# Optimization experiments

Measured on AMD Instinct MI355X. Metric: run time of the kernel, lower is better.

The kernel has to match this reference:

```python
import jax, jax.numpy as jnp
import numpy as np

B, T, D, UNITS, NUM_OUT = 64, 1024, 256, 256, 32


def setup_inputs() -> dict:
    key = jax.random.key(0)
    k1, k2, k3 = jax.random.split(key, 3)
    inputs = jax.random.normal(k1, (B, T, D), dtype=jnp.float32)
    U = jax.random.normal(k2, (D, 4 * UNITS), dtype=jnp.float32) * 0.05
    W = jax.random.normal(k3, (UNITS, 4 * UNITS), dtype=jnp.float32) * 0.05
    b = jnp.zeros((4 * UNITS,), dtype=jnp.float32)
    return {"inputs": inputs, "U": U, "W": W, "b": b, "num_outputs": NUM_OUT}


def reference(inputs, U, W, b, num_outputs):
    # inputs: [B, T, D]; U: [D, 4u]; W: [u, 4u]; b: [4u]
    Bsz, Tlen, _ = inputs.shape
    units = W.shape[0]
    # Precompute input projection as one batched GEMM (x_t @ U + b for all t)
    xz = jnp.einsum('btd,dk->btk', inputs, U) + b  # [B, T, 4u]

    def step(carry, xz_t):
        h, c = carry
        z = xz_t + h @ W  # [B, 4u]
        z0, z1, z2, z3 = jnp.split(z, 4, axis=1)
        i = jax.nn.sigmoid(z0)
        f = jax.nn.sigmoid(z1)
        c_new = f * c + i * jnp.tanh(z2)
        o = jax.nn.sigmoid(z3)
        h_new = o * jnp.tanh(c_new)
        return (h_new, c_new), h_new

    h0 = jnp.zeros((Bsz, units), dtype=inputs.dtype)
    c0 = jnp.zeros((Bsz, units), dtype=inputs.dtype)
    (_, _), hs = jax.lax.scan(step, (h0, c0), jnp.swapaxes(xz, 0, 1))  # hs: [T, B, u]
    outputs = jnp.swapaxes(hs, 0, 1)[:, Tlen - num_outputs:, :]  # [B, num_outputs, u]
    return outputs
```

## Files before the change

### kernel.cpp

```cpp
#include <hip/hip_runtime.h>
#include <hip/hip_fp16.h>
#include <stdint.h>

#define Bsz 64
#define Tsz 1024
#define Dsz 256
#define UNITSn 256
#define Zdim 1024
#define K2n 128
#define WREG 24
#define WLDS 8

typedef _Float16 half2v __attribute__((ext_vector_type(2)));

__device__ __forceinline__ float dot2acc(uint32_t w, uint32_t h, float acc) {
#if __has_builtin(__builtin_amdgcn_fdot2)
  return __builtin_amdgcn_fdot2(__builtin_bit_cast(half2v, w),
                                __builtin_bit_cast(half2v, h), acc, false);
#else
  __half2 wv = __builtin_bit_cast(__half2, w);
  __half2 hv = __builtin_bit_cast(__half2, h);
  acc = fmaf(__half2float(__low2half(wv)),  __half2float(__low2half(hv)),  acc);
  acc = fmaf(__half2float(__high2half(wv)), __half2float(__high2half(hv)), acc);
  return acc;
#endif
}

__device__ __forceinline__ void dot8(const uint4& w0, const uint4& w1, const uint4& h4,
                                     float& a0, float& a1) {
  a0 = dot2acc(w0.x, h4.x, a0); a0 = dot2acc(w0.y, h4.y, a0);
  a0 = dot2acc(w0.z, h4.z, a0); a0 = dot2acc(w0.w, h4.w, a0);
  a1 = dot2acc(w1.x, h4.x, a1); a1 = dot2acc(w1.y, h4.y, a1);
  a1 = dot2acc(w1.z, h4.z, a1); a1 = dot2acc(w1.w, h4.w, a1);
}

__device__ __forceinline__ float sigm(float x)   { return 1.0f / (1.0f + __expf(-x)); }
__device__ __forceinline__ float tanh_f(float x) { return 1.0f - 2.0f / (__expf(2.0f * x) + 1.0f); }

__global__ void convert_w(const float* __restrict__ W, uint32_t* __restrict__ Wp2) {
  int idx = blockIdx.x * 256 + threadIdx.x;
  if (idx >= Zdim * K2n) return;
  int j = idx >> 7, k2 = idx & 127;
  float w0 = W[(size_t)(2 * k2) * Zdim + j];
  float w1 = W[(size_t)(2 * k2 + 1) * Zdim + j];
  __half2 p = __floats2half2_rn(w0, w1);
  Wp2[idx] = __builtin_bit_cast(uint32_t, p);
}

__global__ __launch_bounds__(256) void proj_gemm(
    const float* __restrict__ x, const float* __restrict__ U,
    const float* __restrict__ bias, float* __restrict__ xz, int t0) {
  __shared__ float At[32][68];
  __shared__ float Bt[32][68];
  const int tid  = threadIdx.x;
  const int n0   = blockIdx.x * 64;
  const int tloc = blockIdx.y;
  const int t    = t0 + tloc;
  const int tm = tid >> 4, tn = tid & 15;
  const int am = tid >> 3, ak = (tid & 7) * 4;
  const int bk = tid >> 4, bn = (tid & 15) * 4;
  const float* xb = x + (size_t)t * Dsz;

  float acc[4][4] = {};
  for (int k0 = 0; k0 < Dsz; k0 += 32) {
    float4 a0 = *(const float4*)(xb + (size_t)am * (Tsz * Dsz) + k0 + ak);
    float4 a1 = *(const float4*)(xb + (size_t)(am + 32) * (Tsz * Dsz) + k0 + ak);
    float4 b0 = *(const float4*)(U + (size_t)(k0 + bk) * Zdim + n0 + bn);
    float4 b1 = *(const float4*)(U + (size_t)(k0 + bk + 16) * Zdim + n0 + bn);
    __syncthreads();
    At[ak + 0][am] = a0.x; At[ak + 1][am] = a0.y; At[ak + 2][am] = a0.z; At[ak + 3][am] = a0.w;
    At[ak + 0][am + 32] = a1.x; At[ak + 1][am + 32] = a1.y; At[ak + 2][am + 32] = a1.z; At[ak + 3][am + 32] = a1.w;
    *(float4*)&Bt[bk][bn]      = b0;
    *(float4*)&Bt[bk + 16][bn] = b1;
    __syncthreads();
#pragma unroll
    for (int kk = 0; kk < 32; kk++) {
      float4 av = *(const float4*)&At[kk][tm * 4];
      float4 bv = *(const float4*)&Bt[kk][tn * 4];
      float a_[4] = {av.x, av.y, av.z, av.w};
      float b_[4] = {bv.x, bv.y, bv.z, bv.w};
#pragma unroll
      for (int i = 0; i < 4; i++)
#pragma unroll
        for (int j = 0; j < 4; j++) acc[i][j] = fmaf(a_[i], b_[j], acc[i][j]);
    }
  }
  float4 bb = *(const float4*)&bias[n0 + tn * 4];
  float bias_[4] = {bb.x, bb.y, bb.z, bb.w};
#pragma unroll
  for (int i = 0; i < 4; i++) {
    float4 o;
    o.x = acc[i][0] + bias_[0]; o.y = acc[i][1] + bias_[1];
    o.z = acc[i][2] + bias_[2]; o.w = acc[i][3] + bias_[3];
    *(float4*)(xz + ((size_t)tloc * 64 + tm * 4 + i) * Zdim + n0 + tn * 4) = o;
  }
}

__global__ __launch_bounds__(512, 2) void lstm_chunk(
    const float* __restrict__ xz, const uint32_t* __restrict__ Wp2,
    float* __restrict__ out, uint4* __restrict__ h_state, float* __restrict__ c_state,
    int t0, int Tc, int n_out) {
  extern __shared__ uint32_t smem[];
  uint32_t* Wl = smem;
  uint4* hq    = (uint4*)(smem + 32768);
  float* zf    = (float*)(smem + 32768 + 256);
  float* zo    = zf + 256;

  const int tid = threadIdx.x;
  const int b   = blockIdx.x;

  const uint4* wp0 = (const uint4*)(Wp2 + (size_t)tid * K2n);
  const uint4* wp1 = (const uint4*)(Wp2 + (size_t)(tid + 512) * K2n);
  uint4 w4[2][WREG];
#pragma unroll
  for (int i = 0; i < WREG; i++) { w4[0][i] = wp0[i]; w4[1][i] = wp1[i]; }
#pragma unroll
  for (int q2 = 0; q2 < WLDS; q2++) {
    *(uint4*)(Wl + (size_t)(q2 * 512 + tid) * 4)          = wp0[WREG + q2];
    *(uint4*)(Wl + (size_t)((WLDS + q2) * 512 + tid) * 4) = wp1[WREG + q2];
  }

  float c = 0.0f;
  if (t0 == 0) {
    if (tid < 64) hq[tid] = make_uint4(0, 0, 0, 0);
  } else {
    if (tid < 32)  hq[tid] = h_state[(size_t)b * 32 + tid];
    if (tid < 256) c = c_state[(size_t)b * 256 + tid];
  }
  __syncthreads();

  const float* xzb = xz + (size_t)b * Zdim;
  float nx0 = xzb[tid];
  float nx1 = xzb[tid + 512];
  for (int tl = 0; tl < Tc; tl++) {
    const int buf = tl & 1;
    float acc0 = nx0, acc1 = nx1;
    if (tl + 1 < Tc) {
      nx0 = xzb[(size_t)(tl + 1) * (Bsz * Zdim) + tid];
      nx1 = xzb[(size_t)(tl + 1) * (Bsz * Zdim) + tid + 512];
    }
    const uint4* hc = hq + buf * 32;
#pragma unroll
    for (int q = 0; q < WREG; q++) {
      uint4 h4 = hc[q];
      dot8(w4[0][q], w4[1][q], h4, acc0, acc1);
    }
#pragma unroll
    for (int q2 = 0; q2 < WLDS; q2++) {
      uint4 h4 = hc[WREG + q2];
      uint4 wa = *(const uint4*)(Wl + (size_t)(q2 * 512 + tid) * 4);
      uint4 wb = *(const uint4*)(Wl + (size_t)((WLDS + q2) * 512 + tid) * 4);
      dot8(wa, wb, h4, acc0, acc1);
    }
    if (tid >= 256) { zf[tid - 256] = acc0; zo[tid - 256] = acc1; }
    __syncthreads();
    if (tid < 256) {
      float ig = sigm(acc0);
      float gg = tanh_f(acc1);
      float fg = sigm(zf[tid]);
      float og = sigm(zo[tid]);
      c = fg * c + ig * gg;
      float hn = og * tanh_f(c);
      int ot = (t0 + tl) - (Tsz - n_out);
      if (ot >= 0) out[((size_t)b * n_out + ot) * UNITSn + tid] = hn;
      ((__half*)(hq + (buf ^ 1) * 32))[tid] = __float2half(hn);
    }
    __syncthreads();
  }
  if (tid < 32)  h_state[(size_t)b * 32 + tid] = hq[(Tc & 1) * 32 + tid];
  if (tid < 256) c_state[(size_t)b * 256 + tid] = c;
}

extern "C" void kernel_launch(void* const* d_in, const int* in_sizes, int n_in,
                              void* d_out, int out_size, void* d_ws, size_t ws_size,
                              hipStream_t stream) {
  const float* x    = (const float*)d_in[0];
  const float* U    = (const float*)d_in[1];
  const float* W    = (const float*)d_in[2];
  const float* bias = (const float*)d_in[3];
  float* out = (float*)d_out;
  const int n_out = out_size / (Bsz * UNITSn);

  uint8_t* ws = (uint8_t*)d_ws;
  uint32_t* Wp2  = (uint32_t*)ws;
  uint4* h_state = (uint4*)(ws + (512u << 10));
  float* c_state = (float*)(ws + (544u << 10));
  float* xz      = (float*)(ws + (1u << 20));

  int Tc = Tsz;
  while (Tc > 1 && (size_t)(1u << 20) + (size_t)Tc * (Bsz * Zdim) * 4 > ws_size) Tc >>= 1;

  convert_w<<<dim3((Zdim * K2n + 255) / 256), dim3(256), 0, stream>>>(W, Wp2);

  const int ldsBytes = (32768 + 256 + 512) * 4;
  hipFuncSetAttribute((const void*)lstm_chunk,
                      hipFuncAttributeMaxDynamicSharedMemorySize, ldsBytes);

  for (int t0 = 0; t0 < Tsz; t0 += Tc) {
    proj_gemm<<<dim3(16, Tc), dim3(256), 0, stream>>>(x, U, bias, xz, t0);
    lstm_chunk<<<dim3(Bsz), dim3(512), ldsBytes, stream>>>(xz, Wp2, out, h_state,
                                                           c_state, t0, Tc, n_out);
  }
}
```

Before: 2.055 ms.

## Split recurrent matvec across K halves with register and global-cached weight tiers

```diff
diff --git a/kernel.cpp b/kernel.cpp
--- a/kernel.cpp
+++ b/kernel.cpp
@@ -7,9 +7,8 @@
 #define Dsz 256
 #define UNITSn 256
 #define Zdim 1024
-#define K2n 128
-#define WREG 24
-#define WLDS 8
+#define QV 12
+#define QG 4
 
 typedef _Float16 half2v __attribute__((ext_vector_type(2)));
 
@@ -26,25 +25,47 @@
 #endif
 }
 
-__device__ __forceinline__ void dot8(const uint4& w0, const uint4& w1, const uint4& h4,
-                                     float& a0, float& a1) {
-  a0 = dot2acc(w0.x, h4.x, a0); a0 = dot2acc(w0.y, h4.y, a0);
-  a0 = dot2acc(w0.z, h4.z, a0); a0 = dot2acc(w0.w, h4.w, a0);
-  a1 = dot2acc(w1.x, h4.x, a1); a1 = dot2acc(w1.y, h4.y, a1);
-  a1 = dot2acc(w1.z, h4.z, a1); a1 = dot2acc(w1.w, h4.w, a1);
+__device__ __forceinline__ float dot4(const uint4& w, const uint4& h, float acc) {
+  acc = dot2acc(w.x, h.x, acc); acc = dot2acc(w.y, h.y, acc);
+  acc = dot2acc(w.z, h.z, acc); acc = dot2acc(w.w, h.w, acc);
+  return acc;
 }
 
 __device__ __forceinline__ float sigm(float x)   { return 1.0f / (1.0f + __expf(-x)); }
 __device__ __forceinline__ float tanh_f(float x) { return 1.0f - 2.0f / (__expf(2.0f * x) + 1.0f); }
 
-__global__ void convert_w(const float* __restrict__ W, uint32_t* __restrict__ Wp2) {
-  int idx = blockIdx.x * 256 + threadIdx.x;
-  if (idx >= Zdim * K2n) return;
-  int j = idx >> 7, k2 = idx & 127;
-  float w0 = W[(size_t)(2 * k2) * Zdim + j];
-  float w1 = W[(size_t)(2 * k2 + 1) * Zdim + j];
-  __half2 p = __floats2half2_rn(w0, w1);
-  Wp2[idx] = __builtin_bit_cast(uint32_t, p);
+__global__ __launch_bounds__(256) void convert_w2(const float* __restrict__ W,
+                                                  uint4* __restrict__ Wreg,
+                                                  uint4* __restrict__ Wg) {
+  int i = blockIdx.x * 256 + threadIdx.x;
+  if (i >= 512 * (QV + QG) * 4) return;
+  bool isReg = i < 512 * QV * 4;
+  int q, t, k2rel, col;
+  if (isReg) {
+    q = i >> 9; t = i & 511;
+    int g = q / QV, j = q - g * QV;
+    k2rel = j * 4;
+    col = g * 256 + (t & 255);
+  } else {
+    int i2 = i - 512 * QV * 4;
+    q = i2 >> 9; t = i2 & 511;
+    int g = q >> 2, jj = q & 3;
+    k2rel = QV * 4 + jj * 4;
+    col = g * 256 + (t & 255);
+  }
+  int half = t >> 8;
+  uint32_t d[4];
+#pragma unroll
+  for (int e = 0; e < 4; e++) {
+    int k2 = half * 64 + k2rel + e;
+    float w0 = W[(size_t)(2 * k2) * Zdim + col];
+    float w1 = W[(size_t)(2 * k2 + 1) * Zdim + col];
+    __half2 p = __floats2half2_rn(w0, w1);
+    d[e] = __builtin_bit_cast(uint32_t, p);
+  }
+  uint4 v = make_uint4(d[0], d[1], d[2], d[3]);
+  if (isReg) Wreg[(size_t)q * 512 + t] = v;
+  else       Wg[(size_t)q * 512 + t] = v;
 }
 
 __global__ __launch_bounds__(256) void proj_gemm(
@@ -96,79 +117,81 @@
   }
 }
 
-__global__ __launch_bounds__(512, 2) void lstm_chunk(
-    const float* __restrict__ xz, const uint32_t* __restrict__ Wp2,
-    float* __restrict__ out, uint4* __restrict__ h_state, float* __restrict__ c_state,
+__global__ __launch_bounds__(512, 1) void lstm_chunk(
+    const float* __restrict__ xz, const uint4* __restrict__ Wreg,
+    const uint4* __restrict__ Wg, float* __restrict__ out,
+    uint4* __restrict__ h_state, float* __restrict__ c_state,
     int t0, int Tc, int n_out) {
-  extern __shared__ uint32_t smem[];
-  uint32_t* Wl = smem;
-  uint4* hq    = (uint4*)(smem + 32768);
-  float* zf    = (float*)(smem + 32768 + 256);
-  float* zo    = zf + 256;
-
-  const int tid = threadIdx.x;
-  const int b   = blockIdx.x;
-
-  const uint4* wp0 = (const uint4*)(Wp2 + (size_t)tid * K2n);
-  const uint4* wp1 = (const uint4*)(Wp2 + (size_t)(tid + 512) * K2n);
-  uint4 w4[2][WREG];
-#pragma unroll
-  for (int i = 0; i < WREG; i++) { w4[0][i] = wp0[i]; w4[1][i] = wp1[i]; }
-#pragma unroll
-  for (int q2 = 0; q2 < WLDS; q2++) {
-    *(uint4*)(Wl + (size_t)(q2 * 512 + tid) * 4)          = wp0[WREG + q2];
-    *(uint4*)(Wl + (size_t)((WLDS + q2) * 512 + tid) * 4) = wp1[WREG + q2];
-  }
+  __shared__ uint4 hq4[2][32];
+  __shared__ float4 ppL[256];
+  const int tid  = threadIdx.x;
+  const int b    = blockIdx.x;
+  const int half = tid >> 8, u = tid & 255;
+
+  uint4 wr[4][QV];
+#pragma unroll
+  for (int g = 0; g < 4; g++)
+#pragma unroll
+    for (int j = 0; j < QV; j++)
+      wr[g][j] = Wreg[(size_t)(g * QV + j) * 512 + tid];
 
   float c = 0.0f;
   if (t0 == 0) {
-    if (tid < 64) hq[tid] = make_uint4(0, 0, 0, 0);
+    if (tid < 64) ((uint4*)hq4)[tid] = make_uint4(0, 0, 0, 0);
   } else {
-    if (tid < 32)  hq[tid] = h_state[(size_t)b * 32 + tid];
-    if (tid < 256) c = c_state[(size_t)b * 256 + tid];
+    if (tid < 32)  ((uint4*)hq4)[tid] = h_state[(size_t)b * 32 + tid];
+    if (half == 0) c = c_state[(size_t)b * 256 + u];
   }
   __syncthreads();
 
-  const float* xzb = xz + (size_t)b * Zdim;
-  float nx0 = xzb[tid];
-  float nx1 = xzb[tid + 512];
+  const float* xzb = xz + (size_t)b * Zdim + u;
+  float nx0 = 0, nx1 = 0, nx2 = 0, nx3 = 0;
+  if (half == 0) { nx0 = xzb[0]; nx1 = xzb[256]; nx2 = xzb[512]; nx3 = xzb[768]; }
+  const uint4* wgt = Wg + tid;
+
   for (int tl = 0; tl < Tc; tl++) {
     const int buf = tl & 1;
-    float acc0 = nx0, acc1 = nx1;
-    if (tl + 1 < Tc) {
-      nx0 = xzb[(size_t)(tl + 1) * (Bsz * Zdim) + tid];
-      nx1 = xzb[(size_t)(tl + 1) * (Bsz * Zdim) + tid + 512];
+    const uint4* hb = hq4[buf] + half * 16;
+    float a0 = 0, a1 = 0, a2 = 0, a3 = 0;
+    uint4 l0 = wgt[0 * 512], l1 = wgt[1 * 512], l2 = wgt[2 * 512], l3 = wgt[3 * 512];
+    uint4 l4 = wgt[4 * 512], l5 = wgt[5 * 512], l6 = wgt[6 * 512], l7 = wgt[7 * 512];
+#pragma unroll
+    for (int j = 0; j < QV; j++) {
+      uint4 h4 = hb[j];
+      a0 = dot4(wr[0][j], h4, a0);
+      a1 = dot4(wr[1][j], h4, a1);
+      a2 = dot4(wr[2][j], h4, a2);
+      a3 = dot4(wr[3][j], h4, a3);
     }
-    const uint4* hc = hq + buf * 32;
-#pragma unroll
-    for (int q = 0; q < WREG; q++) {
-      uint4 h4 = hc[q];
-      dot8(w4[0][q], w4[1][q], h4, acc0, acc1);
-    }
-#pragma unroll
-    for (int q2 = 0; q2 < WLDS; q2++) {
-      uint4 h4 = hc[WREG + q2];
-      uint4 wa = *(const uint4*)(Wl + (size_t)(q2 * 512 + tid) * 4);
-      uint4 wb = *(const uint4*)(Wl + (size_t)((WLDS + q2) * 512 + tid) * 4);
-      dot8(wa, wb, h4, acc0, acc1);
-    }
-    if (tid >= 256) { zf[tid - 256] = acc0; zo[tid - 256] = acc1; }
-    __syncthreads();
-    if (tid < 256) {
-      float ig = sigm(acc0);
-      float gg = tanh_f(acc1);
-      float fg = sigm(zf[tid]);
-      float og = sigm(zo[tid]);
+    uint4 hg0 = hb[QV + 0], hg1 = hb[QV + 1], hg2 = hb[QV + 2], hg3 = hb[QV + 3];
+    a0 = dot4(l0, hg0, a0); a0 = dot4(l1, hg1, a0); a0 = dot4(l2, hg2, a0); a0 = dot4(l3, hg3, a0);
+    a1 = dot4(l4, hg0, a1); a1 = dot4(l5, hg1, a1); a1 = dot4(l6, hg2, a1); a1 = dot4(l7, hg3, a1);
+    uint4 m0 = wgt[8 * 512],  m1 = wgt[9 * 512],  m2 = wgt[10 * 512], m3 = wgt[11 * 512];
+    uint4 m4 = wgt[12 * 512], m5 = wgt[13 * 512], m6 = wgt[14 * 512], m7 = wgt[15 * 512];
+    a2 = dot4(m0, hg0, a2); a2 = dot4(m1, hg1, a2); a2 = dot4(m2, hg2, a2); a2 = dot4(m3, hg3, a2);
+    a3 = dot4(m4, hg0, a3); a3 = dot4(m5, hg1, a3); a3 = dot4(m6, hg2, a3); a3 = dot4(m7, hg3, a3);
+
+    if (half) ppL[u] = make_float4(a0, a1, a2, a3);
+    __syncthreads();
+    if (!half) {
+      float4 pp = ppL[u];
+      float z0 = a0 + pp.x + nx0, z1 = a1 + pp.y + nx1;
+      float z2 = a2 + pp.z + nx2, z3 = a3 + pp.w + nx3;
+      if (tl + 1 < Tc) {
+        const float* xn = xzb + (size_t)(tl + 1) * (Bsz * Zdim);
+        nx0 = xn[0]; nx1 = xn[256]; nx2 = xn[512]; nx3 = xn[768];
+      }
+      float ig = sigm(z0), fg = sigm(z1), gg = tanh_f(z2), og = sigm(z3);
       c = fg * c + ig * gg;
       float hn = og * tanh_f(c);
       int ot = (t0 + tl) - (Tsz - n_out);
-      if (ot >= 0) out[((size_t)b * n_out + ot) * UNITSn + tid] = hn;
-      ((__half*)(hq + (buf ^ 1) * 32))[tid] = __float2half(hn);
+      if (ot >= 0) out[((size_t)b * n_out + ot) * UNITSn + u] = hn;
+      ((__half*)hq4[buf ^ 1])[u] = __float2half(hn);
     }
     __syncthreads();
   }
-  if (tid < 32)  h_state[(size_t)b * 32 + tid] = hq[(Tc & 1) * 32 + tid];
-  if (tid < 256) c_state[(size_t)b * 256 + tid] = c;
+  if (tid < 32)  h_state[(size_t)b * 32 + tid] = ((uint4*)hq4)[(Tc & 1) * 32 + tid];
+  if (half == 0) c_state[(size_t)b * 256 + u] = c;
 }
 
 extern "C" void kernel_launch(void* const* d_in, const int* in_sizes, int n_in,
@@ -182,7 +205,8 @@
   const int n_out = out_size / (Bsz * UNITSn);
 
   uint8_t* ws = (uint8_t*)d_ws;
-  uint32_t* Wp2  = (uint32_t*)ws;
+  uint4* Wreg    = (uint4*)ws;
+  uint4* Wg      = (uint4*)(ws + (384u << 10));
   uint4* h_state = (uint4*)(ws + (512u << 10));
   float* c_state = (float*)(ws + (544u << 10));
   float* xz      = (float*)(ws + (1u << 20));
@@ -190,15 +214,11 @@
   int Tc = Tsz;
   while (Tc > 1 && (size_t)(1u << 20) + (size_t)Tc * (Bsz * Zdim) * 4 > ws_size) Tc >>= 1;
 
-  convert_w<<<dim3((Zdim * K2n + 255) / 256), dim3(256), 0, stream>>>(W, Wp2);
-
-  const int ldsBytes = (32768 + 256 + 512) * 4;
-  hipFuncSetAttribute((const void*)lstm_chunk,
-                      hipFuncAttributeMaxDynamicSharedMemorySize, ldsBytes);
+  convert_w2<<<dim3(128), dim3(256), 0, stream>>>(W, Wreg, Wg);
 
   for (int t0 = 0; t0 < Tsz; t0 += Tc) {
     proj_gemm<<<dim3(16, Tc), dim3(256), 0, stream>>>(x, U, bias, xz, t0);
-    lstm_chunk<<<dim3(Bsz), dim3(512), ldsBytes, stream>>>(xz, Wp2, out, h_state,
-                                                           c_state, t0, Tc, n_out);
-  }
-}
+    lstm_chunk<<<dim3(Bsz), dim3(512), 0, stream>>>(xz, Wreg, Wg, out, h_state,
+                                                    c_state, t0, Tc, n_out);
+  }
+}
```

New measurement: 3.522 ms. +71.4%, slower.
